# Optimization experiments

Hardware: AMD Instinct MI355X
Metric: run time of the kernel (lower is better)

Reference implementation:

```python
import jax, jax.numpy as jnp
import numpy as np

N_GRIDS = 16
N_FEATS = 2
GRID_SHAPE = (64, 64, 64)  # D, H, W
NODES = 64
N_OUT = 1
DATA_MIN = 0.0
DATA_MAX = 1.0
N_POINTS = 524288


def setup_inputs() -> dict:
    key = jax.random.key(0)
    ks = jax.random.split(key, 12)
    x = jax.random.uniform(ks[0], (N_POINTS, 3), jnp.float32, -1.0, 1.0)
    # matches randomize_grids(): scales ~ log(1 - U*0.05), rotations ~ identity quat + noise,
    # translations ~ U(-0.05, 0.05)
    scales = jnp.log(1.0 - jax.random.uniform(ks[1], (N_GRIDS, 3), jnp.float32) * 0.05)
    rotations = jnp.zeros((N_GRIDS, 4), jnp.float32).at[:, 3].set(1.0) \
        + jax.random.normal(ks[2], (N_GRIDS, 4), jnp.float32) * 0.05
    translations = jax.random.uniform(ks[3], (N_GRIDS, 3), jnp.float32) * 0.1 - 0.05
    # original uses U(-1e-4, 1e-4); use a larger scale for numerically meaningful outputs
    feature_grids = jax.random.uniform(ks[4], (N_GRIDS, N_FEATS) + GRID_SHAPE,
                                       jnp.float32, -0.1, 0.1)
    d_in = N_GRIDS * N_FEATS
    def xavier(k, fi, fo):
        std = np.sqrt(2.0 / (fi + fo)).astype(np.float32)
        return jax.random.normal(k, (fi, fo), jnp.float32) * std
    W0 = xavier(ks[5], d_in, NODES)
    b0 = jax.random.normal(ks[6], (NODES,), jnp.float32) * 0.001
    W1 = xavier(ks[7], NODES, NODES)
    b1 = jax.random.normal(ks[8], (NODES,), jnp.float32) * 0.001
    W2 = xavier(ks[9], NODES, N_OUT)
    b2 = jax.random.normal(ks[10], (N_OUT,), jnp.float32) * 0.001
    return {"x": x, "rotations": rotations, "scales": scales,
            "translations": translations, "feature_grids": feature_grids,
            "W0": W0, "b0": b0, "W1": W1, "b1": b1, "W2": W2, "b2": b2}


def quat_to_rot(q):
    # q: [G,4] in (x, y, z, w) order; normalized (rotation_activation)
    q = q / jnp.linalg.norm(q, axis=-1, keepdims=True)
    x, y, z, w = q[:, 0], q[:, 1], q[:, 2], q[:, 3]
    r0 = jnp.stack([1 - 2 * (y * y + z * z), 2 * (x * y - z * w), 2 * (x * z + y * w)], -1)
    r1 = jnp.stack([2 * (x * y + z * w), 1 - 2 * (x * x + z * z), 2 * (y * z - x * w)], -1)
    r2 = jnp.stack([2 * (x * z - y * w), 2 * (y * z + x * w), 1 - 2 * (x * x + y * y)], -1)
    return jnp.stack([r0, r1, r2], axis=-2)  # [G,3,3]


def transform_points(x, rotations, scales, translations):
    # S*R*T order: local = diag(exp(scales)) @ R @ x + t, per grid -> [G,N,3]
    R = quat_to_rot(rotations)
    s = jnp.exp(scales)
    M = s[:, :, None] * R  # [G,3,3]
    return jnp.einsum('gij,nj->gni', M, x) + translations[:, None, :]


def trilinear_sample(grid, pts):
    # grid: [C,D,H,W]; pts: [N,3] (x,y,z) in [-1,1]; grid_sample semantics:
    # mode='bilinear', align_corners=True, padding_mode='zeros'
    C, D, H, W = grid.shape
    fx = (pts[:, 0] + 1.0) * 0.5 * (W - 1)
    fy = (pts[:, 1] + 1.0) * 0.5 * (H - 1)
    fz = (pts[:, 2] + 1.0) * 0.5 * (D - 1)
    x0 = jnp.floor(fx); y0 = jnp.floor(fy); z0 = jnp.floor(fz)
    wx = fx - x0; wy = fy - y0; wz = fz - z0
    x0i = x0.astype(jnp.int32); y0i = y0.astype(jnp.int32); z0i = z0.astype(jnp.int32)

    def corner(dx, dy, dz):
        xi = x0i + dx; yi = y0i + dy; zi = z0i + dz
        valid = (xi >= 0) & (xi < W) & (yi >= 0) & (yi < H) & (zi >= 0) & (zi < D)
        v = grid[:, jnp.clip(zi, 0, D - 1), jnp.clip(yi, 0, H - 1), jnp.clip(xi, 0, W - 1)]
        w = ((wx if dx else 1 - wx) * (wy if dy else 1 - wy) * (wz if dz else 1 - wz))
        return v * jnp.where(valid, w, 0.0)[None, :]

    out = corner(0, 0, 0)
    for dz in (0, 1):
        for dy in (0, 1):
            for dx in (0, 1):
                if (dx, dy, dz) != (0, 0, 0):
                    out = out + corner(dx, dy, dz)
    return out  # [C,N]


def reference(x, rotations, scales, translations, feature_grids, W0, b0, W1, b1, W2, b2):
    pts = transform_points(x, rotations, scales, translations)      # [G,N,3]
    feats = jax.vmap(trilinear_sample)(feature_grids, pts)          # [G,C,N]
    feats = feats.transpose(2, 0, 1).reshape(x.shape[0], -1)        # [N, G*C]
    h = jax.nn.relu(feats @ W0 + b0)
    h = jax.nn.relu(h @ W1 + b1)
    y = h @ W2 + b2
    return y * (DATA_MAX - DATA_MIN) + DATA_MIN
```

## Files before the change

kernel.cpp:

```cpp
#include <hip/hip_runtime.h>
#include <cstddef>
#include <cstdint>

constexpr int NPTS   = 524288;
constexpr int NG     = 16;
constexpr int GR     = 64;
constexpr int GR3    = GR * GR * GR;
constexpr int NNODES = 64;
constexpr int NBINS  = 32768;

constexpr size_t GRIDS_BYTES = (size_t)NG * GR3 * 8;
constexpr size_t WS_SORT     = GRIDS_BYTES;
constexpr size_t SORT_BYTES  = (size_t)NPTS * 16;
constexpr size_t WS_KEYR     = WS_SORT + SORT_BYTES;
constexpr size_t KEYR_BYTES  = (size_t)NPTS * 4;
constexpr size_t WS_BINS     = WS_KEYR + KEYR_BYTES;
constexpr size_t BINS_BYTES  = (size_t)NBINS * 4;
constexpr size_t WS_MATS     = WS_BINS + BINS_BYTES;
constexpr size_t MATS_BYTES  = 1024;
constexpr size_t WS_WPACK    = WS_MATS + MATS_BYTES;
constexpr size_t WPACK_BYTES = (size_t)(256 + 512) * 16;
constexpr size_t WS_TOTAL    = WS_WPACK + WPACK_BYTES;

typedef _Float16 half8 __attribute__((ext_vector_type(8)));
typedef float    floatx4 __attribute__((ext_vector_type(4)));

__device__ __forceinline__ unsigned part1by2(unsigned x) {
    x &= 0x3ff;
    x = (x | (x << 16)) & 0x030000FF;
    x = (x | (x <<  8)) & 0x0300F00F;
    x = (x | (x <<  4)) & 0x030C30C3;
    x = (x | (x <<  2)) & 0x09249249;
    return x;
}

__device__ __forceinline__ unsigned cell_of(float px, float py, float pz) {
    int cx = (int)((px + 1.0f) * 16.0f); cx = min(max(cx, 0), 31);
    int cy = (int)((py + 1.0f) * 16.0f); cy = min(max(cy, 0), 31);
    int cz = (int)((pz + 1.0f) * 16.0f); cz = min(max(cz, 0), 31);
    return part1by2((unsigned)cx) | (part1by2((unsigned)cy) << 1) | (part1by2((unsigned)cz) << 2);
}

__device__ __forceinline__ unsigned f32_to_bf16_rne(float f) {
    unsigned u = __float_as_uint(f);
    return (u + 0x7fffu + ((u >> 16) & 1u)) >> 16;
}

__device__ __forceinline__ unsigned pack_h2(float a, float b) {
    unsigned short ua = __builtin_bit_cast(unsigned short, (_Float16)a);
    unsigned short ub = __builtin_bit_cast(unsigned short, (_Float16)b);
    return (unsigned)ua | ((unsigned)ub << 16);
}

__global__ __launch_bounds__(64) void precompute_mats(const float* __restrict__ rot,
                                                      const float* __restrict__ scl,
                                                      const float* __restrict__ trn,
                                                      float* __restrict__ mats) {
    const int g = threadIdx.x;
    if (g >= NG) return;
    float qx = rot[g*4+0], qy = rot[g*4+1], qz = rot[g*4+2], qw = rot[g*4+3];
    const float inv = 1.0f / sqrtf(qx*qx + qy*qy + qz*qz + qw*qw);
    qx *= inv; qy *= inv; qz *= inv; qw *= inv;
    const float sx = expf(scl[g*3+0]);
    const float sy = expf(scl[g*3+1]);
    const float sz = expf(scl[g*3+2]);
    float* m = mats + g * 12;
    m[0] = sx * (1.0f - 2.0f*(qy*qy + qz*qz));
    m[1] = sx * (2.0f*(qx*qy - qz*qw));
    m[2] = sx * (2.0f*(qx*qz + qy*qw));
    m[3] = sy * (2.0f*(qx*qy + qz*qw));
    m[4] = sy * (1.0f - 2.0f*(qx*qx + qz*qz));
    m[5] = sy * (2.0f*(qy*qz - qx*qw));
    m[6] = sz * (2.0f*(qx*qz - qy*qw));
    m[7] = sz * (2.0f*(qy*qz + qx*qw));
    m[8] = sz * (1.0f - 2.0f*(qx*qx + qy*qy));
    m[9]  = trn[g*3+0];
    m[10] = trn[g*3+1];
    m[11] = trn[g*3+2];
}

__global__ __launch_bounds__(256) void pack_weights(const float* __restrict__ W0,
                                                    const float* __restrict__ W1,
                                                    uint4* __restrict__ wpack) {
    const int tid = threadIdx.x;
    const int t = tid >> 6;
    const int lane = tid & 63;
    const int q = lane >> 4, c = lane & 15;
    const int n = t * 16 + c;
    {
        unsigned u[4];
        #pragma unroll
        for (int jj = 0; jj < 4; ++jj) {
            const int k0 = q * 8 + 2 * jj;
            u[jj] = pack_h2(W0[k0 * NNODES + n], W0[(k0 + 1) * NNODES + n]);
        }
        wpack[t * 64 + lane] = make_uint4(u[0], u[1], u[2], u[3]);
    }
    #pragma unroll
    for (int ks = 0; ks < 2; ++ks) {
        unsigned u[4];
        #pragma unroll
        for (int jj = 0; jj < 4; ++jj) {
            const int k0 = ks * 32 + q * 8 + 2 * jj;
            u[jj] = pack_h2(W1[k0 * NNODES + n], W1[(k0 + 1) * NNODES + n]);
        }
        wpack[256 + (ks * 4 + t) * 64 + lane] = make_uint4(u[0], u[1], u[2], u[3]);
    }
}

__global__ __launch_bounds__(256) void repack_grids(const float* __restrict__ grids,
                                                    uint2* __restrict__ gout) {
    const int node = blockIdx.x * 256 + threadIdx.x;
    const int g = blockIdx.y;
    const int x = node & 63;
    const float* base = grids + (size_t)g * 2 * GR3;
    const int nodep = (x < 63) ? node + 1 : node;
    const float c0 = base[node],  c1 = base[GR3 + node];
    const float d0 = base[nodep], d1 = base[GR3 + nodep];
    gout[(size_t)g * GR3 + node] =
        make_uint2(f32_to_bf16_rne(c0) | (f32_to_bf16_rne(c1) << 16),
                   f32_to_bf16_rne(d0) | (f32_to_bf16_rne(d1) << 16));
}

__global__ __launch_bounds__(256) void hist_kernel(const float* __restrict__ xs,
                                                   unsigned* __restrict__ bins,
                                                   unsigned* __restrict__ keyrank) {
    const int n = blockIdx.x * 256 + threadIdx.x;
    if (n >= NPTS) return;
    const unsigned key = cell_of(xs[n*3+0], xs[n*3+1], xs[n*3+2]);
    const unsigned rank = atomicAdd(&bins[key], 1u);
    keyrank[n] = key | (rank << 15);
}

__global__ __launch_bounds__(1024) void scan_kernel(unsigned* __restrict__ bins) {
    __shared__ unsigned s[1024];
    const int t = threadIdx.x;
    unsigned loc[32];
    unsigned sum = 0;
    #pragma unroll
    for (int i = 0; i < 32; ++i) { loc[i] = bins[t * 32 + i]; sum += loc[i]; }
    s[t] = sum;
    __syncthreads();
    for (int off = 1; off < 1024; off <<= 1) {
        unsigned v = (t >= off) ? s[t - off] : 0u;
        __syncthreads();
        s[t] += v;
        __syncthreads();
    }
    unsigned run = s[t] - sum;
    #pragma unroll
    for (int i = 0; i < 32; ++i) { bins[t * 32 + i] = run; run += loc[i]; }
}

__global__ __launch_bounds__(256) void scatter_kernel(const float* __restrict__ xs,
                                                      const unsigned* __restrict__ bins,
                                                      const unsigned* __restrict__ keyrank,
                                                      float4* __restrict__ sorted) {
    const int n = blockIdx.x * 256 + threadIdx.x;
    if (n >= NPTS) return;
    const unsigned kr = keyrank[n];
    const unsigned key = kr & 0x7fffu;
    const unsigned rank = kr >> 15;
    const unsigned pos = bins[key] + rank;
    sorted[pos] = make_float4(xs[n*3+0], xs[n*3+1], xs[n*3+2], __int_as_float(n));
}

struct Geom {
    int i00, i01, i10, i11;
    float ax0, ax1, ay0, ay1, az0, az1;
    unsigned selhi, sello;
};

__device__ __forceinline__ Geom make_geom(const float* __restrict__ m,
                                          float px, float py, float pz, int g) {
    Geom G;
    const float tx = fmaf(m[0], px, fmaf(m[1], py, fmaf(m[2], pz, m[9])));
    const float ty = fmaf(m[3], px, fmaf(m[4], py, fmaf(m[5], pz, m[10])));
    const float tz = fmaf(m[6], px, fmaf(m[7], py, fmaf(m[8], pz, m[11])));
    const float fx = (tx + 1.0f) * 31.5f;
    const float fy = (ty + 1.0f) * 31.5f;
    const float fz = (tz + 1.0f) * 31.5f;
    const float x0f = floorf(fx), y0f = floorf(fy), z0f = floorf(fz);
    const float wx = fx - x0f, wy = fy - y0f, wz = fz - z0f;
    const int x0 = (int)x0f, y0 = (int)y0f, z0 = (int)z0f;
    G.ax0 = ((unsigned)x0       < 64u) ? (1.0f - wx) : 0.0f;
    G.ax1 = ((unsigned)(x0 + 1) < 64u) ? wx          : 0.0f;
    G.ay0 = ((unsigned)y0       < 64u) ? (1.0f - wy) : 0.0f;
    G.ay1 = ((unsigned)(y0 + 1) < 64u) ? wy          : 0.0f;
    G.az0 = ((unsigned)z0       < 64u) ? (1.0f - wz) : 0.0f;
    G.az1 = ((unsigned)(z0 + 1) < 64u) ? wz          : 0.0f;
    G.selhi = (x0 >= 63) ? 1u : 0u;
    G.sello = (x0 <= -1) ? 1u : 0u;
    const int xb  = min(max(x0, 0), 62);
    const int yc0 = min(max(y0, 0), 63),     yc1 = min(max(y0 + 1, 0), 63);
    const int zc0 = min(max(z0, 0), 63),     zc1 = min(max(z0 + 1, 0), 63);
    const int b = (g << 18) + xb;
    G.i00 = b + (zc0 << 12) + (yc0 << 6);
    G.i01 = b + (zc0 << 12) + (yc1 << 6);
    G.i10 = b + (zc1 << 12) + (yc0 << 6);
    G.i11 = b + (zc1 << 12) + (yc1 << 6);
    return G;
}

__device__ __forceinline__ void acc_pair(float& f0, float& f1, const Geom& G,
                                         uint2 q, float wyz) {
    const unsigned v0 = G.selhi ? q.y : q.x;
    const unsigned v1 = G.sello ? q.x : q.y;
    float s0 = G.ax0 * __uint_as_float(v0 << 16);
    s0 = fmaf(G.ax1, __uint_as_float(v1 << 16), s0);
    f0 = fmaf(wyz, s0, f0);
    float s1 = G.ax0 * __uint_as_float(v0 & 0xffff0000u);
    s1 = fmaf(G.ax1, __uint_as_float(v1 & 0xffff0000u), s1);
    f1 = fmaf(wyz, s1, f1);
}

constexpr int ARENA_H = 64 * 66;
constexpr int FSTRIDE = 40;

__global__ __launch_bounds__(256, 3) void amgsrn_main(
    const float4* __restrict__ sorted,
    const uint2*  __restrict__ gridsP,
    const float*  __restrict__ mats,
    const uint4*  __restrict__ wpack,
    const float*  __restrict__ b0,
    const float*  __restrict__ b1,
    const float*  __restrict__ W2,
    const float*  __restrict__ b2,
    float* __restrict__ out)
{
    __shared__ unsigned short sh[4 * ARENA_H];
    __shared__ float yS[256];

    const int tid  = threadIdx.x;
    const int lane = tid & 63;
    const int wv   = tid >> 6;
    const int c    = lane & 15;
    const int q    = lane >> 4;
    unsigned short* wa = sh + wv * ARENA_H;

    const int n = blockIdx.x * 256 + tid;
    const float4 p = sorted[n];
    const float px = p.x, py = p.y, pz = p.z;
    const int orig = __float_as_int(p.w);

    unsigned pk[NG];
    Geom G = make_geom(mats, px, py, pz, 0);
    uint2 q00 = gridsP[G.i00], q01 = gridsP[G.i01];
    uint2 q10 = gridsP[G.i10], q11 = gridsP[G.i11];
    #pragma unroll
    for (int g = 0; g < NG; ++g) {
        Geom Gn;
        uint2 n00, n01, n10, n11;
        if (g + 1 < NG) {
            Gn = make_geom(mats + (g + 1) * 12, px, py, pz, g + 1);
            n00 = gridsP[Gn.i00]; n01 = gridsP[Gn.i01];
            n10 = gridsP[Gn.i10]; n11 = gridsP[Gn.i11];
        }
        float f0 = 0.0f, f1 = 0.0f;
        acc_pair(f0, f1, G, q00, G.az0 * G.ay0);
        acc_pair(f0, f1, G, q01, G.az0 * G.ay1);
        acc_pair(f0, f1, G, q10, G.az1 * G.ay0);
        acc_pair(f0, f1, G, q11, G.az1 * G.ay1);
        pk[g] = pack_h2(f0, f1);
        if (g + 1 < NG) {
            G = Gn;
            q00 = n00; q01 = n01; q10 = n10; q11 = n11;
        }
    }

    {
        uint4* dst = (uint4*)(wa + lane * FSTRIDE);
        dst[0] = make_uint4(pk[0],  pk[1],  pk[2],  pk[3]);
        dst[1] = make_uint4(pk[4],  pk[5],  pk[6],  pk[7]);
        dst[2] = make_uint4(pk[8],  pk[9],  pk[10], pk[11]);
        dst[3] = make_uint4(pk[12], pk[13], pk[14], pk[15]);
    }
    __syncthreads();

    half8 a0[4];
    #pragma unroll
    for (int m = 0; m < 4; ++m)
        a0[m] = *(const half8*)(wa + (m * 16 + c) * FSTRIDE + q * 8);

    half8 b0f[4], b1f[2][4];
    #pragma unroll
    for (int t = 0; t < 4; ++t)
        b0f[t] = __builtin_bit_cast(half8, wpack[t * 64 + lane]);
    #pragma unroll
    for (int ks = 0; ks < 2; ++ks)
        #pragma unroll
        for (int t = 0; t < 4; ++t)
            b1f[ks][t] = __builtin_bit_cast(half8, wpack[256 + (ks * 4 + t) * 64 + lane]);
    float b0v[4], b1v[4], w2v[4];
    #pragma unroll
    for (int t = 0; t < 4; ++t) {
        b0v[t] = b0[t * 16 + c];
        b1v[t] = b1[t * 16 + c];
        w2v[t] = W2[t * 16 + c];
    }
    const float b2s = b2[0];

    __syncthreads();

    #pragma unroll
    for (int t = 0; t < 4; ++t) {
        #pragma unroll
        for (int m = 0; m < 4; ++m) {
            floatx4 acc = {b0v[t], b0v[t], b0v[t], b0v[t]};
            acc = __builtin_amdgcn_mfma_f32_16x16x32_f16(a0[m], b0f[t], acc, 0, 0, 0);
            const int node = t * 16 + c;
            const int pt   = m * 16 + q * 4;
            unsigned* w32 = (unsigned*)(wa + node * 66 + pt);
            w32[0] = pack_h2(fmaxf(acc[0], 0.0f), fmaxf(acc[1], 0.0f));
            w32[1] = pack_h2(fmaxf(acc[2], 0.0f), fmaxf(acc[3], 0.0f));
        }
    }
    __syncthreads();

    half8 a1[4][2];
    #pragma unroll
    for (int m = 0; m < 4; ++m) {
        #pragma unroll
        for (int ks = 0; ks < 2; ++ks) {
            unsigned u[4];
            #pragma unroll
            for (int jj = 0; jj < 4; ++jj) {
                const int k0 = ks * 32 + q * 8 + 2 * jj;
                const unsigned lo = wa[k0 * 66 + m * 16 + c];
                const unsigned hi = wa[(k0 + 1) * 66 + m * 16 + c];
                u[jj] = lo | (hi << 16);
            }
            a1[m][ks] = __builtin_bit_cast(half8, make_uint4(u[0], u[1], u[2], u[3]));
        }
    }

    float p4[4][4];
    #pragma unroll
    for (int m = 0; m < 4; ++m)
        #pragma unroll
        for (int r = 0; r < 4; ++r) p4[m][r] = 0.0f;

    #pragma unroll
    for (int t = 0; t < 4; ++t) {
        #pragma unroll
        for (int m = 0; m < 4; ++m) {
            floatx4 acc = {b1v[t], b1v[t], b1v[t], b1v[t]};
            acc = __builtin_amdgcn_mfma_f32_16x16x32_f16(a1[m][0], b1f[0][t], acc, 0, 0, 0);
            acc = __builtin_amdgcn_mfma_f32_16x16x32_f16(a1[m][1], b1f[1][t], acc, 0, 0, 0);
            #pragma unroll
            for (int r = 0; r < 4; ++r)
                p4[m][r] = fmaf(fmaxf(acc[r], 0.0f), w2v[t], p4[m][r]);
        }
    }

    #pragma unroll
    for (int m = 0; m < 4; ++m)
        #pragma unroll
        for (int r = 0; r < 4; ++r) {
            float v = p4[m][r];
            v += __shfl_xor(v, 1, 64);
            v += __shfl_xor(v, 2, 64);
            v += __shfl_xor(v, 4, 64);
            v += __shfl_xor(v, 8, 64);
            p4[m][r] = v + b2s;
        }

    if (c == 0) {
        #pragma unroll
        for (int m = 0; m < 4; ++m)
            #pragma unroll
            for (int r = 0; r < 4; ++r)
                yS[wv * 64 + m * 16 + q * 4 + r] = p4[m][r];
    }
    __syncthreads();
    out[orig] = yS[tid];
}

__global__ __launch_bounds__(256, 3) void amgsrn_fused_fallback(
    const float* __restrict__ xs,
    const float* __restrict__ rot,
    const float* __restrict__ scl,
    const float* __restrict__ trn,
    const float* __restrict__ grids,
    const float* __restrict__ W0,
    const float* __restrict__ b0,
    const float* __restrict__ W1,
    const float* __restrict__ b1,
    const float* __restrict__ W2,
    const float* __restrict__ b2,
    float* __restrict__ out)
{
    __shared__ float sM[NG][12];
    const int tid = threadIdx.x;
    if (tid < NG) {
        const int g = tid;
        float qx = rot[g*4+0], qy = rot[g*4+1], qz = rot[g*4+2], qw = rot[g*4+3];
        const float inv = 1.0f / sqrtf(qx*qx + qy*qy + qz*qz + qw*qw);
        qx *= inv; qy *= inv; qz *= inv; qw *= inv;
        const float sx = expf(scl[g*3+0]);
        const float sy = expf(scl[g*3+1]);
        const float sz = expf(scl[g*3+2]);
        sM[g][0] = sx * (1.0f - 2.0f*(qy*qy + qz*qz));
        sM[g][1] = sx * (2.0f*(qx*qy - qz*qw));
        sM[g][2] = sx * (2.0f*(qx*qz + qy*qw));
        sM[g][3] = sy * (2.0f*(qx*qy + qz*qw));
        sM[g][4] = sy * (1.0f - 2.0f*(qx*qx + qz*qz));
        sM[g][5] = sy * (2.0f*(qy*qz - qx*qw));
        sM[g][6] = sz * (2.0f*(qx*qz - qy*qw));
        sM[g][7] = sz * (2.0f*(qy*qz + qx*qw));
        sM[g][8] = sz * (1.0f - 2.0f*(qx*qx + qy*qy));
        sM[g][9]  = trn[g*3+0];
        sM[g][10] = trn[g*3+1];
        sM[g][11] = trn[g*3+2];
    }
    __syncthreads();

    const int n = blockIdx.x * blockDim.x + tid;
    if (n >= NPTS) return;
    const float px = xs[n*3+0];
    const float py = xs[n*3+1];
    const float pz = xs[n*3+2];

    float h0[NNODES];
    #pragma unroll
    for (int j = 0; j < NNODES; ++j) h0[j] = b0[j];

    #pragma unroll
    for (int g = 0; g < NG; ++g) {
        const float* m = sM[g];
        const float tx = m[0]*px + m[1]*py + m[2]*pz + m[9];
        const float ty = m[3]*px + m[4]*py + m[5]*pz + m[10];
        const float tz = m[6]*px + m[7]*py + m[8]*pz + m[11];
        const float fx = (tx + 1.0f) * 31.5f;
        const float fy = (ty + 1.0f) * 31.5f;
        const float fz = (tz + 1.0f) * 31.5f;
        const float x0f = floorf(fx), y0f = floorf(fy), z0f = floorf(fz);
        const float wx = fx - x0f, wy = fy - y0f, wz = fz - z0f;
        const int x0 = (int)x0f, y0 = (int)y0f, z0 = (int)z0f;
        const float* gb = grids + (size_t)g * (size_t)(2 * GR3);
        float f0 = 0.0f, f1 = 0.0f;
        #pragma unroll
        for (int dz = 0; dz < 2; ++dz) {
            #pragma unroll
            for (int dy = 0; dy < 2; ++dy) {
                #pragma unroll
                for (int dx = 0; dx < 2; ++dx) {
                    const int xi = x0 + dx, yi = y0 + dy, zi = z0 + dz;
                    const bool valid = ((unsigned)xi < (unsigned)GR) &
                                       ((unsigned)yi < (unsigned)GR) &
                                       ((unsigned)zi < (unsigned)GR);
                    const int xc = min(max(xi, 0), GR-1);
                    const int yc = min(max(yi, 0), GR-1);
                    const int zc = min(max(zi, 0), GR-1);
                    float w = (dx ? wx : 1.0f - wx) *
                              (dy ? wy : 1.0f - wy) *
                              (dz ? wz : 1.0f - wz);
                    w = valid ? w : 0.0f;
                    const int idx = (zc * GR + yc) * GR + xc;
                    f0 = fmaf(w, gb[idx], f0);
                    f1 = fmaf(w, gb[idx + GR3], f1);
                }
            }
        }
        const float* w0a = W0 + (2*g    ) * NNODES;
        const float* w0b = W0 + (2*g + 1) * NNODES;
        #pragma unroll
        for (int j = 0; j < NNODES; ++j)
            h0[j] = fmaf(f1, w0b[j], fmaf(f0, w0a[j], h0[j]));
    }
    #pragma unroll
    for (int j = 0; j < NNODES; ++j) h0[j] = fmaxf(h0[j], 0.0f);

    float y = b2[0];
    #pragma unroll
    for (int half = 0; half < 2; ++half) {
        float h1[32];
        #pragma unroll
        for (int j = 0; j < 32; ++j) h1[j] = b1[half * 32 + j];
        #pragma unroll
        for (int k = 0; k < NNODES; ++k) {
            const float a = h0[k];
            const float* w = W1 + k * NNODES + half * 32;
            #pragma unroll
            for (int j = 0; j < 32; ++j) h1[j] = fmaf(a, w[j], h1[j]);
        }
        #pragma unroll
        for (int j = 0; j < 32; ++j) y = fmaf(fmaxf(h1[j], 0.0f), W2[half * 32 + j], y);
    }

    out[n] = y;
}

extern "C" void kernel_launch(void* const* d_in, const int* in_sizes, int n_in,
                              void* d_out, int out_size, void* d_ws, size_t ws_size,
                              hipStream_t stream) {
    const float* xs  = (const float*)d_in[0];
    const float* rot = (const float*)d_in[1];
    const float* scl = (const float*)d_in[2];
    const float* trn = (const float*)d_in[3];
    const float* gr  = (const float*)d_in[4];
    const float* W0  = (const float*)d_in[5];
    const float* b0  = (const float*)d_in[6];
    const float* W1  = (const float*)d_in[7];
    const float* b1  = (const float*)d_in[8];
    const float* W2  = (const float*)d_in[9];
    const float* b2  = (const float*)d_in[10];
    float* out = (float*)d_out;

    if (ws_size < WS_TOTAL) {
        dim3 grid((NPTS + 255) / 256), block(256);
        hipLaunchKernelGGL(amgsrn_fused_fallback, grid, block, 0, stream,
                           xs, rot, scl, trn, gr, W0, b0, W1, b1, W2, b2, out);
        return;
    }

    char* ws = (char*)d_ws;
    uint2*    gridsP  = (uint2*)(ws);
    float4*   sorted  = (float4*)(ws + WS_SORT);
    unsigned* keyrank = (unsigned*)(ws + WS_KEYR);
    unsigned* bins    = (unsigned*)(ws + WS_BINS);
    float*    mats    = (float*)(ws + WS_MATS);
    uint4*    wpack   = (uint4*)(ws + WS_WPACK);

    hipLaunchKernelGGL(precompute_mats, dim3(1), dim3(64), 0, stream,
                       rot, scl, trn, mats);
    hipLaunchKernelGGL(pack_weights, dim3(1), dim3(256), 0, stream,
                       W0, W1, wpack);
    hipLaunchKernelGGL(repack_grids, dim3(GR3 / 256, NG), dim3(256), 0, stream,
                       gr, gridsP);
    hipMemsetAsync(bins, 0, BINS_BYTES, stream);
    hipLaunchKernelGGL(hist_kernel, dim3((NPTS + 255) / 256), dim3(256), 0, stream,
                       xs, bins, keyrank);
    hipLaunchKernelGGL(scan_kernel, dim3(1), dim3(1024), 0, stream, bins);
    hipLaunchKernelGGL(scatter_kernel, dim3((NPTS + 255) / 256), dim3(256), 0, stream,
                       xs, bins, keyrank, sorted);
    hipLaunchKernelGGL(amgsrn_main, dim3(NPTS / 256), dim3(256), 0, stream,
                       sorted, gridsP, mats, wpack, b0, b1, W2, b2, out);
}
```

Before: 197.3 us.

## Fuse preprocessing kernels into one launch, vectorize grid repack, raise occupancy

Merges the matrix precompute, weight packing, grid repack and histogram kernels into a single prep kernel that picks its role from the block index. This removes several launches and lets the independent preprocessing jobs run at the same time. The grid repack now handles four nodes per thread with float4 loads and 16-byte stores. The main kernel's launch bounds rise from 3 to 4 blocks per CU, which may force register spills.

```diff
diff --git a/kernel.cpp b/kernel.cpp
--- a/kernel.cpp
+++ b/kernel.cpp
@@ -22,6 +22,9 @@
 constexpr size_t WPACK_BYTES = (size_t)(256 + 512) * 16;
 constexpr size_t WS_TOTAL    = WS_WPACK + WPACK_BYTES;
 
+constexpr int PREP_REPACK = 4096;
+constexpr int PREP_HIST   = 2048;
+
 typedef _Float16 half8 __attribute__((ext_vector_type(8)));
 typedef float    floatx4 __attribute__((ext_vector_type(4)));
 
@@ -52,84 +55,92 @@
     return (unsigned)ua | ((unsigned)ub << 16);
 }
 
-__global__ __launch_bounds__(64) void precompute_mats(const float* __restrict__ rot,
-                                                      const float* __restrict__ scl,
-                                                      const float* __restrict__ trn,
-                                                      float* __restrict__ mats) {
-    const int g = threadIdx.x;
-    if (g >= NG) return;
-    float qx = rot[g*4+0], qy = rot[g*4+1], qz = rot[g*4+2], qw = rot[g*4+3];
-    const float inv = 1.0f / sqrtf(qx*qx + qy*qy + qz*qz + qw*qw);
-    qx *= inv; qy *= inv; qz *= inv; qw *= inv;
-    const float sx = expf(scl[g*3+0]);
-    const float sy = expf(scl[g*3+1]);
-    const float sz = expf(scl[g*3+2]);
-    float* m = mats + g * 12;
-    m[0] = sx * (1.0f - 2.0f*(qy*qy + qz*qz));
-    m[1] = sx * (2.0f*(qx*qy - qz*qw));
-    m[2] = sx * (2.0f*(qx*qz + qy*qw));
-    m[3] = sy * (2.0f*(qx*qy + qz*qw));
-    m[4] = sy * (1.0f - 2.0f*(qx*qx + qz*qz));
-    m[5] = sy * (2.0f*(qy*qz - qx*qw));
-    m[6] = sz * (2.0f*(qx*qz - qy*qw));
-    m[7] = sz * (2.0f*(qy*qz + qx*qw));
-    m[8] = sz * (1.0f - 2.0f*(qx*qx + qy*qy));
-    m[9]  = trn[g*3+0];
-    m[10] = trn[g*3+1];
-    m[11] = trn[g*3+2];
-}
-
-__global__ __launch_bounds__(256) void pack_weights(const float* __restrict__ W0,
-                                                    const float* __restrict__ W1,
-                                                    uint4* __restrict__ wpack) {
+__global__ __launch_bounds__(256) void prep_kernel(
+    const float* __restrict__ grids, uint2* __restrict__ gout,
+    const float* __restrict__ xs, unsigned* __restrict__ bins,
+    unsigned* __restrict__ keyrank,
+    const float* __restrict__ rot, const float* __restrict__ scl,
+    const float* __restrict__ trn, float* __restrict__ mats,
+    const float* __restrict__ W0, const float* __restrict__ W1,
+    uint4* __restrict__ wpack)
+{
+    const int bid = blockIdx.x;
     const int tid = threadIdx.x;
-    const int t = tid >> 6;
-    const int lane = tid & 63;
-    const int q = lane >> 4, c = lane & 15;
-    const int n = t * 16 + c;
-    {
-        unsigned u[4];
-        #pragma unroll
-        for (int jj = 0; jj < 4; ++jj) {
-            const int k0 = q * 8 + 2 * jj;
-            u[jj] = pack_h2(W0[k0 * NNODES + n], W0[(k0 + 1) * NNODES + n]);
-        }
-        wpack[t * 64 + lane] = make_uint4(u[0], u[1], u[2], u[3]);
-    }
-    #pragma unroll
-    for (int ks = 0; ks < 2; ++ks) {
-        unsigned u[4];
-        #pragma unroll
-        for (int jj = 0; jj < 4; ++jj) {
-            const int k0 = ks * 32 + q * 8 + 2 * jj;
-            u[jj] = pack_h2(W1[k0 * NNODES + n], W1[(k0 + 1) * NNODES + n]);
-        }
-        wpack[256 + (ks * 4 + t) * 64 + lane] = make_uint4(u[0], u[1], u[2], u[3]);
-    }
-}
-
-__global__ __launch_bounds__(256) void repack_grids(const float* __restrict__ grids,
-                                                    uint2* __restrict__ gout) {
-    const int node = blockIdx.x * 256 + threadIdx.x;
-    const int g = blockIdx.y;
-    const int x = node & 63;
-    const float* base = grids + (size_t)g * 2 * GR3;
-    const int nodep = (x < 63) ? node + 1 : node;
-    const float c0 = base[node],  c1 = base[GR3 + node];
-    const float d0 = base[nodep], d1 = base[GR3 + nodep];
-    gout[(size_t)g * GR3 + node] =
-        make_uint2(f32_to_bf16_rne(c0) | (f32_to_bf16_rne(c1) << 16),
-                   f32_to_bf16_rne(d0) | (f32_to_bf16_rne(d1) << 16));
-}
-
-__global__ __launch_bounds__(256) void hist_kernel(const float* __restrict__ xs,
-                                                   unsigned* __restrict__ bins,
-                                                   unsigned* __restrict__ keyrank) {
-    const int n = blockIdx.x * 256 + threadIdx.x;
-    if (n >= NPTS) return;
-    const unsigned key = cell_of(xs[n*3+0], xs[n*3+1], xs[n*3+2]);
-    const unsigned rank = atomicAdd(&bins[key], 1u);
-    keyrank[n] = key | (rank << 15);
+
+    if (bid < PREP_REPACK) {
+        const int base = (bid * 256 + tid) * 4;
+        const int g    = base >> 18;
+        const int node = base & (GR3 - 1);
+        const int x    = node & 63;
+        const float* p0 = grids + (size_t)g * 2 * GR3 + node;
+        const float* p1 = p0 + GR3;
+        const float4 c0 = *(const float4*)p0;
+        const float4 c1 = *(const float4*)p1;
+        float d0n, d1n;
+        if (x == 60) { d0n = c0.w; d1n = c1.w; }
+        else         { d0n = p0[4]; d1n = p1[4]; }
+        const float e0[5] = {c0.x, c0.y, c0.z, c0.w, d0n};
+        const float e1[5] = {c1.x, c1.y, c1.z, c1.w, d1n};
+        unsigned pk[5];
+        #pragma unroll
+        for (int i = 0; i < 5; ++i)
+            pk[i] = f32_to_bf16_rne(e0[i]) | (f32_to_bf16_rne(e1[i]) << 16);
+        uint4* dst = (uint4*)(gout + (size_t)g * GR3 + node);
+        dst[0] = make_uint4(pk[0], pk[1], pk[1], pk[2]);
+        dst[1] = make_uint4(pk[2], pk[3], pk[3], pk[4]);
+    } else if (bid < PREP_REPACK + PREP_HIST) {
+        const int n = (bid - PREP_REPACK) * 256 + tid;
+        const unsigned key = cell_of(xs[n*3+0], xs[n*3+1], xs[n*3+2]);
+        const unsigned rank = atomicAdd(&bins[key], 1u);
+        keyrank[n] = key | (rank << 15);
+    } else if (bid == PREP_REPACK + PREP_HIST) {
+        const int g = tid;
+        if (g < NG) {
+            float qx = rot[g*4+0], qy = rot[g*4+1], qz = rot[g*4+2], qw = rot[g*4+3];
+            const float inv = 1.0f / sqrtf(qx*qx + qy*qy + qz*qz + qw*qw);
+            qx *= inv; qy *= inv; qz *= inv; qw *= inv;
+            const float sx = expf(scl[g*3+0]);
+            const float sy = expf(scl[g*3+1]);
+            const float sz = expf(scl[g*3+2]);
+            float* m = mats + g * 12;
+            m[0] = sx * (1.0f - 2.0f*(qy*qy + qz*qz));
+            m[1] = sx * (2.0f*(qx*qy - qz*qw));
+            m[2] = sx * (2.0f*(qx*qz + qy*qw));
+            m[3] = sy * (2.0f*(qx*qy + qz*qw));
+            m[4] = sy * (1.0f - 2.0f*(qx*qx + qz*qz));
+            m[5] = sy * (2.0f*(qy*qz - qx*qw));
+            m[6] = sz * (2.0f*(qx*qz - qy*qw));
+            m[7] = sz * (2.0f*(qy*qz + qx*qw));
+            m[8] = sz * (1.0f - 2.0f*(qx*qx + qy*qy));
+            m[9]  = trn[g*3+0];
+            m[10] = trn[g*3+1];
+            m[11] = trn[g*3+2];
+        }
+    } else {
+        const int t = tid >> 6;
+        const int lane = tid & 63;
+        const int q = lane >> 4, c = lane & 15;
+        const int n = t * 16 + c;
+        {
+            unsigned u[4];
+            #pragma unroll
+            for (int jj = 0; jj < 4; ++jj) {
+                const int k0 = q * 8 + 2 * jj;
+                u[jj] = pack_h2(W0[k0 * NNODES + n], W0[(k0 + 1) * NNODES + n]);
+            }
+            wpack[t * 64 + lane] = make_uint4(u[0], u[1], u[2], u[3]);
+        }
+        #pragma unroll
+        for (int ks = 0; ks < 2; ++ks) {
+            unsigned u[4];
+            #pragma unroll
+            for (int jj = 0; jj < 4; ++jj) {
+                const int k0 = ks * 32 + q * 8 + 2 * jj;
+                u[jj] = pack_h2(W1[k0 * NNODES + n], W1[(k0 + 1) * NNODES + n]);
+            }
+            wpack[256 + (ks * 4 + t) * 64 + lane] = make_uint4(u[0], u[1], u[2], u[3]);
+        }
+    }
 }
 
 __global__ __launch_bounds__(1024) void scan_kernel(unsigned* __restrict__ bins) {
@@ -217,7 +228,7 @@
 constexpr int ARENA_H = 64 * 66;
 constexpr int FSTRIDE = 40;
 
-__global__ __launch_bounds__(256, 3) void amgsrn_main(
+__global__ __launch_bounds__(256, 4) void amgsrn_main(
     const float4* __restrict__ sorted,
     const uint2*  __restrict__ gridsP,
     const float*  __restrict__ mats,
@@ -522,17 +533,12 @@
     float*    mats    = (float*)(ws + WS_MATS);
     uint4*    wpack   = (uint4*)(ws + WS_WPACK);
 
-    hipLaunchKernelGGL(precompute_mats, dim3(1), dim3(64), 0, stream,
-                       rot, scl, trn, mats);
-    hipLaunchKernelGGL(pack_weights, dim3(1), dim3(256), 0, stream,
-                       W0, W1, wpack);
-    hipLaunchKernelGGL(repack_grids, dim3(GR3 / 256, NG), dim3(256), 0, stream,
-                       gr, gridsP);
     hipMemsetAsync(bins, 0, BINS_BYTES, stream);
-    hipLaunchKernelGGL(hist_kernel, dim3((NPTS + 255) / 256), dim3(256), 0, stream,
-                       xs, bins, keyrank);
+    hipLaunchKernelGGL(prep_kernel, dim3(PREP_REPACK + PREP_HIST + 2), dim3(256), 0, stream,
+                       gr, gridsP, xs, bins, keyrank,
+                       rot, scl, trn, mats, W0, W1, wpack);
     hipLaunchKernelGGL(scan_kernel, dim3(1), dim3(1024), 0, stream, bins);
-    hipLaunchKernelGGL(scatter_kernel, dim3((NPTS + 255) / 256), dim3(256), 0, stream,
+    hipLaunchKernelGGL(scatter_kernel, dim3(NPTS / 256), dim3(256), 0, stream,
                        xs, bins, keyrank, sorted);
     hipLaunchKernelGGL(amgsrn_main, dim3(NPTS / 256), dim3(256), 0, stream,
                        sorted, gridsP, mats, wpack, b0, b1, W2, b2, out);
```

New measurement: 196.8 us. No clear change (-0.2%).
